# Optimization experiments

Measured on AMD Instinct MI355X. Metric: run time of the kernel, lower is better.

## Reference

```python
import jax, jax.numpy as jnp
import numpy as np

B, M, D, H = 32, 1024, 768, 256


def setup_inputs() -> dict:
    key = jax.random.key(0)
    k = jax.random.split(key, 6)
    V = jax.random.normal(k[0], (B, M, D), dtype=jnp.float32)
    alpha = jnp.float32(0.5)
    # torch nn.Linear weights: [out, in]
    WV_w = jax.random.normal(k[1], (H, D), dtype=jnp.float32) * (1.0 / np.sqrt(D))
    WV_b = jnp.zeros((H,), dtype=jnp.float32)
    W_conv = jax.random.normal(k[2], (H, H), dtype=jnp.float32) * (1.0 / np.sqrt(H))
    res_w = jax.random.normal(k[3], (H, D), dtype=jnp.float32) * (1.0 / np.sqrt(D))
    res_b = jnp.zeros((H,), dtype=jnp.float32)
    return {"V": V, "alpha": alpha, "WV_w": WV_w, "WV_b": WV_b,
            "W_conv": W_conv, "res_w": res_w, "res_b": res_b}


def reference(V, alpha, WV_w, WV_b, W_conv, res_w, res_b):
    # global feature awareness enhancement: alpha*V + (1-alpha)*mean
    g = jnp.mean(V, axis=1, keepdims=True)            # [B,1,D]
    V_enh = alpha * V + (1.0 - alpha) * g             # [B,M,D]
    # projection (torch Linear: x @ W.T + b)
    Vp = jnp.einsum('bmd,hd->bmh', V_enh, WV_w) + WV_b  # [B,M,H]
    # dynamic incidence matrix: row-softmax of Vp @ Vp.T
    sim = jnp.einsum('bmh,bnh->bmn', Vp, Vp)          # [B,M,M]
    H_TV = jax.nn.softmax(sim, axis=-1)               # [B,M,M]
    # hypergraph convolution: H @ ((H.T @ X) @ W)
    t1 = jnp.einsum('bnm,bnh->bmh', H_TV, Vp)         # H.T @ X -> [B,M,H]
    t2 = jnp.einsum('bmh,hk->bmk', t1, W_conv)        # [B,M,H]
    O = jnp.einsum('bmn,bnh->bmh', H_TV, t2)          # [B,M,H]
    # residual projection + relu
    res = jnp.einsum('bmd,hd->bmh', V, res_w) + res_b  # [B,M,H]
    return jax.nn.relu(O + res)
```

## Files before the change

### kernel.cpp

```cpp
#include <hip/hip_runtime.h>
#include <math.h>


typedef __attribute__((ext_vector_type(8))) short bf16x8;
typedef __attribute__((ext_vector_type(4))) float f32x4;

__device__ __forceinline__ ushort f2b(float f) {
    unsigned u = __float_as_uint(f);
    return (ushort)((u + 0x7fffu + ((u >> 16) & 1u)) >> 16);
}
__device__ __forceinline__ float b2f(ushort u) {
    return __uint_as_float((unsigned)u << 16);
}
__device__ __forceinline__ uint4 pack8(float4 a, float4 b) {
    uint4 r;
    r.x = f2b(a.x) | ((unsigned)f2b(a.y) << 16);
    r.y = f2b(a.z) | ((unsigned)f2b(a.w) << 16);
    r.z = f2b(b.x) | ((unsigned)f2b(b.y) << 16);
    r.w = f2b(b.z) | ((unsigned)f2b(b.w) << 16);
    return r;
}

__device__ __forceinline__ void gl16(const void* g, void* l) {
    __builtin_amdgcn_global_load_lds(
        (__attribute__((address_space(1))) const unsigned*)g,
        (__attribute__((address_space(3))) unsigned*)l, 16, 0, 0);
}

__device__ __forceinline__ void gemm_core(const ushort* __restrict__ A,
                                          const ushort* __restrict__ Bt,
                                          int K, ushort* As, ushort* Bs,
                                          f32x4 acc[4][4]) {
    const int tid = threadIdx.x;
    const int lane = tid & 63;
    const int wave = tid >> 6;
    const int l8 = lane >> 3, l7 = lane & 7;
    const int swz = ((l7 ^ l8) << 4);
    const char* pa[4];
    const char* pb[4];
    ushort* la[4];
    ushort* lb[4];
    #pragma unroll
    for (int i = 0; i < 4; ++i) {
        int r = (wave * 4 + i) * 8 + l8;
        pa[i] = (const char*)A + (size_t)r * (K * 2) + swz;
        pb[i] = (const char*)Bt + (size_t)r * (K * 2) + swz;
        la[i] = As + (wave * 4 + i) * 512;
        lb[i] = Bs + (wave * 4 + i) * 512;
    }
    const int rr = lane & 15;
    const int kq = (lane >> 4) << 4;
    const int mask = (rr & 7) << 4;
    const int c0 = kq ^ mask;
    const int c1 = (64 + kq) ^ mask;
    const int wr = (wave >> 1) * 64, wc = (wave & 1) * 64;
    const int arow0 = (wr + rr) * 128, brow0 = (wc + rr) * 128;

    for (int k0 = 0; k0 < K; k0 += 64) {
        __syncthreads();
        #pragma unroll
        for (int i = 0; i < 4; ++i) {
            gl16(pa[i], la[i]);
            gl16(pb[i], lb[i]);
            pa[i] += 128; pb[i] += 128;
        }
        __syncthreads();
        #pragma unroll
        for (int ks = 0; ks < 2; ++ks) {
            const int cc = ks ? c1 : c0;
            bf16x8 av[4], bv[4];
            #pragma unroll
            for (int i = 0; i < 4; ++i) {
                av[i] = *(const bf16x8*)((const char*)As + arow0 + i * 2048 + cc);
                bv[i] = *(const bf16x8*)((const char*)Bs + brow0 + i * 2048 + cc);
            }
            #pragma unroll
            for (int i = 0; i < 4; ++i)
                #pragma unroll
                for (int j = 0; j < 4; ++j)
                    acc[i][j] = __builtin_amdgcn_mfma_f32_16x16x32_bf16(av[i], bv[j], acc[i][j], 0, 0, 0);
        }
    }
}

#define EPI_COORDS \
    const int lane = threadIdx.x & 63; \
    const int wave = threadIdx.x >> 6; \
    const int rb = (wave >> 1) * 64 + (lane >> 4) * 4; \
    const int cb = (wave & 1) * 64 + (lane & 15);

__global__ __launch_bounds__(192) void k_castmean(const float* __restrict__ V,
                                                  ushort* __restrict__ Vb,
                                                  float* __restrict__ gpart) {
    const int b = blockIdx.x, mc = blockIdx.y, t = threadIdx.x;
    const size_t base = ((size_t)(b * 1024 + mc * 128)) * 768 + t * 4;
    const float* src = V + base;
    ushort* dst = Vb + base;
    float4 s = make_float4(0.f, 0.f, 0.f, 0.f);
    for (int r = 0; r < 128; ++r) {
        float4 v = *(const float4*)(src + (size_t)r * 768);
        s.x += v.x; s.y += v.y; s.z += v.z; s.w += v.w;
        unsigned u0 = f2b(v.x) | ((unsigned)f2b(v.y) << 16);
        unsigned u1 = f2b(v.z) | ((unsigned)f2b(v.w) << 16);
        *(uint2*)(dst + (size_t)r * 768) = make_uint2(u0, u1);
    }
    *(float4*)&gpart[(size_t)(mc * 32 + b) * 768 + t * 4] = s;
}

__global__ __launch_bounds__(256) void k_gsum(const float* __restrict__ gpart, float* __restrict__ g) {
    int idx = blockIdx.x * 256 + threadIdx.x;
    float s = 0.f;
    #pragma unroll
    for (int c = 0; c < 8; ++c) s += gpart[(size_t)c * 24576 + idx];
    g[idx] = s * (1.0f / 1024.0f);
}

__global__ __launch_bounds__(256) void k_gW(const float* __restrict__ g,
                                            const float* __restrict__ WVw,
                                            float* __restrict__ gW) {
    int idx = blockIdx.x * 256 + threadIdx.x;
    int b = idx >> 8, h = idx & 255;
    const float* gr = g + b * 768;
    const float* wr = WVw + (size_t)h * 768;
    float s = 0.f;
    for (int d = 0; d < 768; ++d) s += gr[d] * wr[d];
    gW[idx] = s;
}

__global__ __launch_bounds__(256) void k_castw(const float* __restrict__ WVw,
                                               const float* __restrict__ resw,
                                               ushort* __restrict__ Wcat) {
    int id = blockIdx.x * 256 + threadIdx.x;
    int n = id / 96, c = (id - n * 96) * 8;
    const float* src = (n < 256) ? (WVw + (size_t)n * 768 + c) : (resw + (size_t)(n - 256) * 768 + c);
    *(uint4*)(Wcat + (size_t)n * 768 + c) = pack8(*(const float4*)src, *(const float4*)(src + 4));
}

__global__ __launch_bounds__(256) void k_wct(const float* __restrict__ Wc, ushort* __restrict__ WcT) {
    __shared__ float t[64][65];
    const int r0 = blockIdx.y * 64, c0 = blockIdx.x * 64;
    const int tid = threadIdx.x;
    #pragma unroll
    for (int i = 0; i < 4; ++i) {
        int r = (tid >> 4) + i * 16, c4 = (tid & 15) * 4;
        float4 v = *(const float4*)&Wc[(size_t)(r0 + r) * 256 + c0 + c4];
        t[r][c4] = v.x; t[r][c4 + 1] = v.y; t[r][c4 + 2] = v.z; t[r][c4 + 3] = v.w;
    }
    __syncthreads();
    #pragma unroll
    for (int i = 0; i < 4; ++i) {
        int oc = (tid >> 4) + i * 16, r4 = (tid & 15) * 4;
        unsigned lo = f2b(t[r4][oc]) | ((unsigned)f2b(t[r4 + 1][oc]) << 16);
        unsigned hi = f2b(t[r4 + 2][oc]) | ((unsigned)f2b(t[r4 + 3][oc]) << 16);
        *(uint2*)&WcT[(size_t)(c0 + oc) * 256 + r0 + r4] = make_uint2(lo, hi);
    }
}

__global__ __launch_bounds__(256) void k_proj(const ushort* __restrict__ Vb, const ushort* __restrict__ Wcat,
                                              const float* __restrict__ WVb, const float* __restrict__ resb,
                                              const float* __restrict__ gW, const float* __restrict__ alpha_p,
                                              ushort* __restrict__ Vp, ushort* __restrict__ resv) {
    __shared__ ushort As[128 * 64], Bs[128 * 64];
    f32x4 acc[4][4] = {};
    const int n0 = blockIdx.x * 128, m0 = blockIdx.y * 128;
    gemm_core(Vb + (size_t)m0 * 768, Wcat + (size_t)n0 * 768, 768, As, Bs, acc);
    EPI_COORDS
    const float alpha = *alpha_p, oma = 1.0f - alpha;
    #pragma unroll
    for (int i = 0; i < 4; ++i)
        #pragma unroll
        for (int j = 0; j < 4; ++j) {
            int gcol = n0 + cb + j * 16;
            #pragma unroll
            for (int r = 0; r < 4; ++r) {
                int grow = m0 + rb + i * 16 + r;
                float v = acc[i][j][r];
                if (gcol < 256) {
                    float o = alpha * v + oma * gW[((grow >> 10) << 8) + gcol] + WVb[gcol];
                    Vp[(size_t)grow * 256 + gcol] = f2b(o);
                } else {
                    resv[(size_t)grow * 256 + gcol - 256] = f2b(v + resb[gcol - 256]);
                }
            }
        }
}

__global__ __launch_bounds__(256) void k_dmax(const ushort* __restrict__ Vp, float* __restrict__ shift) {
    const int b = blockIdx.x;
    const int wave = threadIdx.x >> 6, lane = threadIdx.x & 63;
    const ushort* Vb_ = Vp + (size_t)b * 1024 * 256;
    float mx = -1e30f;
    for (int rr = 0; rr < 256; ++rr) {
        int row = wave * 256 + rr;
        uint2 v = *(const uint2*)(Vb_ + (size_t)row * 256 + lane * 4);
        float f0 = b2f((ushort)(v.x & 0xffff)), f1 = b2f((ushort)(v.x >> 16));
        float f2 = b2f((ushort)(v.y & 0xffff)), f3 = b2f((ushort)(v.y >> 16));
        float s = f0 * f0 + f1 * f1 + f2 * f2 + f3 * f3;
        #pragma unroll
        for (int o = 32; o > 0; o >>= 1) s += __shfl_xor(s, o, 64);
        mx = fmaxf(mx, s);
    }
    __shared__ float red[4];
    if (lane == 0) red[wave] = mx;
    __syncthreads();
    if (threadIdx.x == 0)
        shift[b] = fmaxf(fmaxf(red[0], red[1]), fmaxf(red[2], red[3]));
}

__global__ __launch_bounds__(256) void k_sim(const ushort* __restrict__ Vp,
                                             const float* __restrict__ shift,
                                             ushort* __restrict__ E) {
    __shared__ ushort As[128 * 64], Bs[128 * 64];
    f32x4 acc[4][4] = {};
    const int b = blockIdx.z;
    const ushort* Vb_ = Vp + (size_t)b * 1024 * 256;
    const int n0 = blockIdx.x * 128, m0 = blockIdx.y * 128;
    gemm_core(Vb_ + (size_t)m0 * 256, Vb_ + (size_t)n0 * 256, 256, As, Bs, acc);
    ushort* Eb = E + ((size_t)b << 20);
    const float sh = shift[b];
    EPI_COORDS
    #pragma unroll
    for (int i = 0; i < 4; ++i)
        #pragma unroll
        for (int j = 0; j < 4; ++j)
            #pragma unroll
            for (int r = 0; r < 4; ++r)
                Eb[(size_t)(m0 + rb + i * 16 + r) * 1024 + n0 + cb + j * 16] =
                    f2b(__expf(acc[i][j][r] - sh));
}

__global__ __launch_bounds__(256) void k_rowsum(const ushort* __restrict__ E, float* __restrict__ invZ) {
    const int row = blockIdx.x * 4 + (threadIdx.x >> 6);
    const int lane = threadIdx.x & 63;
    const ushort* p = E + (size_t)row * 1024 + lane * 4;
    float s = 0.f;
    #pragma unroll
    for (int pass = 0; pass < 4; ++pass) {
        uint2 v = *(const uint2*)(p + pass * 256);
        s += b2f((ushort)(v.x & 0xffff)) + b2f((ushort)(v.x >> 16))
           + b2f((ushort)(v.y & 0xffff)) + b2f((ushort)(v.y >> 16));
    }
    #pragma unroll
    for (int o = 32; o > 0; o >>= 1) s += __shfl_xor(s, o, 64);
    if (lane == 0) invZ[row] = 1.0f / s;
}

__global__ __launch_bounds__(256) void k_trbs(const ushort* __restrict__ Vp,
                                              const float* __restrict__ invZ,
                                              ushort* __restrict__ VpZT) {
    __shared__ ushort t[64][68];
    const int b = blockIdx.z;
    const ushort* ib = Vp + (size_t)b * 1024 * 256;
    ushort* ob = VpZT + (size_t)b * 256 * 1024;
    const int c0 = blockIdx.x * 64, r0 = blockIdx.y * 64;
    const int tid = threadIdx.x;
    #pragma unroll
    for (int i = 0; i < 4; ++i) {
        int r = (tid >> 4) + i * 16, c4 = (tid & 15) * 4;
        uint2 v = *(const uint2*)(ib + (size_t)(r0 + r) * 256 + c0 + c4);
        float iz = invZ[b * 1024 + r0 + r];
        unsigned lo = f2b(b2f((ushort)(v.x & 0xffff)) * iz) |
                      ((unsigned)f2b(b2f((ushort)(v.x >> 16)) * iz) << 16);
        unsigned hi = f2b(b2f((ushort)(v.y & 0xffff)) * iz) |
                      ((unsigned)f2b(b2f((ushort)(v.y >> 16)) * iz) << 16);
        *(uint2*)&t[r][c4] = make_uint2(lo, hi);
    }
    __syncthreads();
    #pragma unroll
    for (int i = 0; i < 4; ++i) {
        int oc = (tid >> 4) + i * 16, r4 = (tid & 15) * 4;
        unsigned lo = t[r4][oc] | ((unsigned)t[r4 + 1][oc] << 16);
        unsigned hi = t[r4 + 2][oc] | ((unsigned)t[r4 + 3][oc] << 16);
        *(uint2*)(ob + (size_t)(c0 + oc) * 1024 + r0 + r4) = make_uint2(lo, hi);
    }
}

__global__ __launch_bounds__(256) void k_trb(const ushort* __restrict__ in, ushort* __restrict__ out) {
    __shared__ ushort t[64][68];
    const int b = blockIdx.z;
    const ushort* ib = in + (size_t)b * 1024 * 256;
    ushort* ob = out + (size_t)b * 256 * 1024;
    const int c0 = blockIdx.x * 64, r0 = blockIdx.y * 64;
    const int tid = threadIdx.x;
    #pragma unroll
    for (int i = 0; i < 4; ++i) {
        int r = (tid >> 4) + i * 16, c4 = (tid & 15) * 4;
        *(uint2*)&t[r][c4] = *(const uint2*)(ib + (size_t)(r0 + r) * 256 + c0 + c4);
    }
    __syncthreads();
    #pragma unroll
    for (int i = 0; i < 4; ++i) {
        int oc = (tid >> 4) + i * 16, r4 = (tid & 15) * 4;
        unsigned lo = t[r4][oc] | ((unsigned)t[r4 + 1][oc] << 16);
        unsigned hi = t[r4 + 2][oc] | ((unsigned)t[r4 + 3][oc] << 16);
        *(uint2*)(ob + (size_t)(c0 + oc) * 1024 + r0 + r4) = make_uint2(lo, hi);
    }
}

__global__ __launch_bounds__(256) void k_t1(const ushort* __restrict__ E, const ushort* __restrict__ VpZT,
                                            ushort* __restrict__ t1) {
    __shared__ ushort As[128 * 64], Bs[128 * 64];
    f32x4 acc[4][4] = {};
    const int b = blockIdx.z;
    const int n0 = blockIdx.x * 128, m0 = blockIdx.y * 128;
    gemm_core(E + ((size_t)b << 20) + (size_t)m0 * 1024,
              VpZT + (size_t)b * 256 * 1024 + (size_t)n0 * 1024, 1024, As, Bs, acc);
    ushort* ob = t1 + (size_t)b * 1024 * 256;
    EPI_COORDS
    #pragma unroll
    for (int i = 0; i < 4; ++i)
        #pragma unroll
        for (int j = 0; j < 4; ++j)
            #pragma unroll
            for (int r = 0; r < 4; ++r)
                ob[(size_t)(m0 + rb + i * 16 + r) * 256 + n0 + cb + j * 16] = f2b(acc[i][j][r]);
}

__global__ __launch_bounds__(256) void k_t2(const ushort* __restrict__ t1, const ushort* __restrict__ WcT,
                                            ushort* __restrict__ t2) {
    __shared__ ushort As[128 * 64], Bs[128 * 64];
    f32x4 acc[4][4] = {};
    const int n0 = blockIdx.x * 128, m0 = blockIdx.y * 128;
    gemm_core(t1 + (size_t)m0 * 256, WcT + (size_t)n0 * 256, 256, As, Bs, acc);
    EPI_COORDS
    #pragma unroll
    for (int i = 0; i < 4; ++i)
        #pragma unroll
        for (int j = 0; j < 4; ++j)
            #pragma unroll
            for (int r = 0; r < 4; ++r)
                t2[(size_t)(m0 + rb + i * 16 + r) * 256 + n0 + cb + j * 16] = f2b(acc[i][j][r]);
}

__global__ __launch_bounds__(256) void k_O(const ushort* __restrict__ E, const ushort* __restrict__ t2T,
                                           const ushort* __restrict__ resv, const float* __restrict__ invZ,
                                           float* __restrict__ out) {
    __shared__ ushort As[128 * 64], Bs[128 * 64];
    f32x4 acc[4][4] = {};
    const int b = blockIdx.z;
    const int n0 = blockIdx.x * 128, m0 = blockIdx.y * 128;
    gemm_core(E + ((size_t)b << 20) + (size_t)m0 * 1024,
              t2T + (size_t)b * 256 * 1024 + (size_t)n0 * 1024, 1024, As, Bs, acc);
    EPI_COORDS
    #pragma unroll
    for (int i = 0; i < 4; ++i)
        #pragma unroll
        for (int j = 0; j < 4; ++j)
            #pragma unroll
            for (int r = 0; r < 4; ++r) {
                int row = m0 + rb + i * 16 + r;
                float iz = invZ[b * 1024 + row];
                size_t off = ((size_t)(b * 1024 + row)) * 256 + n0 + cb + j * 16;
                out[off] = fmaxf(acc[i][j][r] * iz + b2f(resv[off]), 0.0f);
            }
}

extern "C" void kernel_launch(void* const* d_in, const int* in_sizes, int n_in,
                              void* d_out, int out_size, void* d_ws, size_t ws_size,
                              hipStream_t stream) {
    const float* V     = (const float*)d_in[0];
    const float* alpha = (const float*)d_in[1];
    const float* WVw   = (const float*)d_in[2];
    const float* WVb   = (const float*)d_in[3];
    const float* Wc    = (const float*)d_in[4];
    const float* resw  = (const float*)d_in[5];
    const float* resb  = (const float*)d_in[6];
    float* out = (float*)d_out;

    char* W = (char*)d_ws;
    ushort* Vb   = (ushort*)(W);
    ushort* E    = (ushort*)(W + (48ull  << 20));
    ushort* Vp   = (ushort*)(W + (112ull << 20));
    ushort* resv = (ushort*)(W + (128ull << 20));
    ushort* VpZT = (ushort*)(W + (144ull << 20));
    ushort* t1   = (ushort*)(W + (160ull << 20));
    ushort* t2   = (ushort*)(W + (176ull << 20));
    ushort* t2T  = (ushort*)(W + (192ull << 20));
    ushort* Wcat = (ushort*)(W + (208ull << 20));
    ushort* WcT  = (ushort*)(W + (209ull << 20));
    float*  gpart= (float*) (W + (210ull << 20));
    float*  g    = (float*) (W + (211ull << 20));
    float*  gW   = (float*) (W + (211ull << 20) + (128u << 10));
    float*  shv  = (float*) (W + (211ull << 20) + (256u << 10));
    float*  invZ = (float*) (W + (212ull << 20));

    k_castmean<<<dim3(32, 8), 192, 0, stream>>>(V, Vb, gpart);
    k_gsum<<<96, 256, 0, stream>>>(gpart, g);
    k_gW<<<32, 256, 0, stream>>>(g, WVw, gW);
    k_castw<<<192, 256, 0, stream>>>(WVw, resw, Wcat);
    k_wct<<<dim3(4, 4), 256, 0, stream>>>(Wc, WcT);
    k_proj<<<dim3(4, 256), 256, 0, stream>>>(Vb, Wcat, WVb, resb, gW, alpha, Vp, resv);
    k_dmax<<<32, 256, 0, stream>>>(Vp, shv);
    k_sim<<<dim3(8, 8, 32), 256, 0, stream>>>(Vp, shv, E);
    k_rowsum<<<8192, 256, 0, stream>>>(E, invZ);
    k_trbs<<<dim3(4, 16, 32), 256, 0, stream>>>(Vp, invZ, VpZT);
    k_t1<<<dim3(2, 8, 32), 256, 0, stream>>>(E, VpZT, t1);
    k_t2<<<dim3(2, 256), 256, 0, stream>>>(t1, WcT, t2);
    k_trb<<<dim3(4, 16, 32), 256, 0, stream>>>(t2, t2T);
    k_O<<<dim3(2, 8, 32), 256, 0, stream>>>(E, t2T, resv, invZ, out);
}
```

Before: 469.4 us.

## Fuse softmax row-sum into sim epilogue via atomics and parallelize row-norm max

Softmax row sums are now accumulated in the sim GEMM epilogue with a 16-lane shuffle reduction plus atomicAdd into a zeroed Z buffer. This removes the separate rowsum kernel that re-read the whole bf16 E matrix. The serial per-batch max-norm kernel, which used only 32 blocks, is split into a row-norm kernel over all rows and a small per-batch max kernel. The cost is a memset, atomic traffic, and summation in fp32 before bf16 rounding, so the row sums differ slightly from the sum of the stored bf16 values.

Result: faster. 416.8 us (-11.2%).

```diff
diff --git a/kernel.cpp b/kernel.cpp
--- a/kernel.cpp
+++ b/kernel.cpp
@@ -185,31 +185,35 @@
         }
 }
 
-__global__ __launch_bounds__(256) void k_dmax(const ushort* __restrict__ Vp, float* __restrict__ shift) {
-    const int b = blockIdx.x;
-    const int wave = threadIdx.x >> 6, lane = threadIdx.x & 63;
-    const ushort* Vb_ = Vp + (size_t)b * 1024 * 256;
-    float mx = -1e30f;
-    for (int rr = 0; rr < 256; ++rr) {
-        int row = wave * 256 + rr;
-        uint2 v = *(const uint2*)(Vb_ + (size_t)row * 256 + lane * 4);
-        float f0 = b2f((ushort)(v.x & 0xffff)), f1 = b2f((ushort)(v.x >> 16));
-        float f2 = b2f((ushort)(v.y & 0xffff)), f3 = b2f((ushort)(v.y >> 16));
-        float s = f0 * f0 + f1 * f1 + f2 * f2 + f3 * f3;
-        #pragma unroll
-        for (int o = 32; o > 0; o >>= 1) s += __shfl_xor(s, o, 64);
-        mx = fmaxf(mx, s);
-    }
+__global__ __launch_bounds__(256) void k_rownorm(const ushort* __restrict__ Vp, float* __restrict__ rn) {
+    const int row = blockIdx.x * 4 + (threadIdx.x >> 6);
+    const int lane = threadIdx.x & 63;
+    uint2 v = *(const uint2*)(Vp + (size_t)row * 256 + lane * 4);
+    float f0 = b2f((ushort)(v.x & 0xffff)), f1 = b2f((ushort)(v.x >> 16));
+    float f2 = b2f((ushort)(v.y & 0xffff)), f3 = b2f((ushort)(v.y >> 16));
+    float s = f0 * f0 + f1 * f1 + f2 * f2 + f3 * f3;
+    #pragma unroll
+    for (int o = 32; o > 0; o >>= 1) s += __shfl_xor(s, o, 64);
+    if (lane == 0) rn[row] = s;
+}
+
+__global__ __launch_bounds__(256) void k_shift(const float* __restrict__ rn, float* __restrict__ shift) {
+    const int b = blockIdx.x, tid = threadIdx.x;
+    const float* p = rn + b * 1024;
+    float m = fmaxf(fmaxf(p[tid], p[tid + 256]), fmaxf(p[tid + 512], p[tid + 768]));
+    #pragma unroll
+    for (int o = 32; o > 0; o >>= 1) m = fmaxf(m, __shfl_xor(m, o, 64));
     __shared__ float red[4];
-    if (lane == 0) red[wave] = mx;
+    if ((tid & 63) == 0) red[tid >> 6] = m;
     __syncthreads();
-    if (threadIdx.x == 0)
+    if (tid == 0)
         shift[b] = fmaxf(fmaxf(red[0], red[1]), fmaxf(red[2], red[3]));
 }
 
 __global__ __launch_bounds__(256) void k_sim(const ushort* __restrict__ Vp,
                                              const float* __restrict__ shift,
-                                             ushort* __restrict__ E) {
+                                             ushort* __restrict__ E,
+                                             float* __restrict__ Z) {
     __shared__ ushort As[128 * 64], Bs[128 * 64];
     f32x4 acc[4][4] = {};
     const int b = blockIdx.z;
@@ -222,31 +226,27 @@
     #pragma unroll
     for (int i = 0; i < 4; ++i)
         #pragma unroll
-        for (int j = 0; j < 4; ++j)
-            #pragma unroll
-            for (int r = 0; r < 4; ++r)
-                Eb[(size_t)(m0 + rb + i * 16 + r) * 1024 + n0 + cb + j * 16] =
-                    f2b(__expf(acc[i][j][r] - sh));
-}
-
-__global__ __launch_bounds__(256) void k_rowsum(const ushort* __restrict__ E, float* __restrict__ invZ) {
-    const int row = blockIdx.x * 4 + (threadIdx.x >> 6);
-    const int lane = threadIdx.x & 63;
-    const ushort* p = E + (size_t)row * 1024 + lane * 4;
-    float s = 0.f;
-    #pragma unroll
-    for (int pass = 0; pass < 4; ++pass) {
-        uint2 v = *(const uint2*)(p + pass * 256);
-        s += b2f((ushort)(v.x & 0xffff)) + b2f((ushort)(v.x >> 16))
-           + b2f((ushort)(v.y & 0xffff)) + b2f((ushort)(v.y >> 16));
-    }
-    #pragma unroll
-    for (int o = 32; o > 0; o >>= 1) s += __shfl_xor(s, o, 64);
-    if (lane == 0) invZ[row] = 1.0f / s;
+        for (int r = 0; r < 4; ++r) {
+            const int row = m0 + rb + i * 16 + r;
+            float e[4];
+            float s = 0.f;
+            #pragma unroll
+            for (int j = 0; j < 4; ++j) {
+                e[j] = __expf(acc[i][j][r] - sh);
+                s += e[j];
+                Eb[(size_t)row * 1024 + n0 + cb + j * 16] = f2b(e[j]);
+            }
+            s += __shfl_xor(s, 1, 64);
+            s += __shfl_xor(s, 2, 64);
+            s += __shfl_xor(s, 4, 64);
+            s += __shfl_xor(s, 8, 64);
+            if ((lane & 15) == 0)
+                atomicAdd(&Z[b * 1024 + row], s);
+        }
 }
 
 __global__ __launch_bounds__(256) void k_trbs(const ushort* __restrict__ Vp,
-                                              const float* __restrict__ invZ,
+                                              const float* __restrict__ Z,
                                               ushort* __restrict__ VpZT) {
     __shared__ ushort t[64][68];
     const int b = blockIdx.z;
@@ -258,7 +258,7 @@
     for (int i = 0; i < 4; ++i) {
         int r = (tid >> 4) + i * 16, c4 = (tid & 15) * 4;
         uint2 v = *(const uint2*)(ib + (size_t)(r0 + r) * 256 + c0 + c4);
-        float iz = invZ[b * 1024 + r0 + r];
+        float iz = 1.0f / Z[b * 1024 + r0 + r];
         unsigned lo = f2b(b2f((ushort)(v.x & 0xffff)) * iz) |
                       ((unsigned)f2b(b2f((ushort)(v.x >> 16)) * iz) << 16);
         unsigned hi = f2b(b2f((ushort)(v.y & 0xffff)) * iz) |
@@ -333,7 +333,7 @@
 }
 
 __global__ __launch_bounds__(256) void k_O(const ushort* __restrict__ E, const ushort* __restrict__ t2T,
-                                           const ushort* __restrict__ resv, const float* __restrict__ invZ,
+                                           const ushort* __restrict__ resv, const float* __restrict__ Z,
                                            float* __restrict__ out) {
     __shared__ ushort As[128 * 64], Bs[128 * 64];
     f32x4 acc[4][4] = {};
@@ -349,7 +349,7 @@
             #pragma unroll
             for (int r = 0; r < 4; ++r) {
                 int row = m0 + rb + i * 16 + r;
-                float iz = invZ[b * 1024 + row];
+                float iz = 1.0f / Z[b * 1024 + row];
                 size_t off = ((size_t)(b * 1024 + row)) * 256 + n0 + cb + j * 16;
                 out[off] = fmaxf(acc[i][j][r] * iz + b2f(resv[off]), 0.0f);
             }
@@ -382,7 +382,10 @@
     float*  g    = (float*) (W + (211ull << 20));
     float*  gW   = (float*) (W + (211ull << 20) + (128u << 10));
     float*  shv  = (float*) (W + (211ull << 20) + (256u << 10));
-    float*  invZ = (float*) (W + (212ull << 20));
+    float*  rn   = (float*) (W + (211ull << 20) + (512u << 10));
+    float*  Z    = (float*) (W + (212ull << 20));
+
+    hipMemsetAsync(Z, 0, 32768 * sizeof(float), stream);
 
     k_castmean<<<dim3(32, 8), 192, 0, stream>>>(V, Vb, gpart);
     k_gsum<<<96, 256, 0, stream>>>(gpart, g);
@@ -390,12 +393,12 @@
     k_castw<<<192, 256, 0, stream>>>(WVw, resw, Wcat);
     k_wct<<<dim3(4, 4), 256, 0, stream>>>(Wc, WcT);
     k_proj<<<dim3(4, 256), 256, 0, stream>>>(Vb, Wcat, WVb, resb, gW, alpha, Vp, resv);
-    k_dmax<<<32, 256, 0, stream>>>(Vp, shv);
-    k_sim<<<dim3(8, 8, 32), 256, 0, stream>>>(Vp, shv, E);
-    k_rowsum<<<8192, 256, 0, stream>>>(E, invZ);
-    k_trbs<<<dim3(4, 16, 32), 256, 0, stream>>>(Vp, invZ, VpZT);
+    k_rownorm<<<8192, 256, 0, stream>>>(Vp, rn);
+    k_shift<<<32, 256, 0, stream>>>(rn, shv);
+    k_sim<<<dim3(8, 8, 32), 256, 0, stream>>>(Vp, shv, E, Z);
+    k_trbs<<<dim3(4, 16, 32), 256, 0, stream>>>(Vp, Z, VpZT);
     k_t1<<<dim3(2, 8, 32), 256, 0, stream>>>(E, VpZT, t1);
     k_t2<<<dim3(2, 256), 256, 0, stream>>>(t1, WcT, t2);
     k_trb<<<dim3(4, 16, 32), 256, 0, stream>>>(t2, t2T);
-    k_O<<<dim3(2, 8, 32), 256, 0, stream>>>(E, t2T, resv, invZ, out);
-}
+    k_O<<<dim3(2, 8, 32), 256, 0, stream>>>(E, t2T, resv, Z, out);
+}
```
